# Optimization experiments

Hardware: AMD Instinct MI355X
Metric: run time of the kernel (lower is better)

The kernel has to match this reference:

```python
import math
import jax, jax.numpy as jnp
import numpy as np

BLOCK = 32          # hard-coded in the CUDA kernels
NUM_HEADS = 16
NUM_BLOCKS = 512    # (max_pos//32) * block_per_row = 128 * 4
DIAG_N = 3
FIRST_N = 0


def _mra2_attention(Q, K, V, mask):
    # Q,K,V: (meta_batch, seq, head_dim); mask: (meta_batch, seq) in {0,1}
    mb, seq_len, d = Q.shape
    bs = BLOCK
    nb = seq_len // bs
    scale = 1.0 / math.sqrt(d)
    Q = Q * mask[:, :, None]
    K = K * mask[:, :, None]
    V = V * mask[:, :, None]

    # ---- low resolution block means (mask-weighted), approx_mode='full' keeps V_hat
    tc = mask.reshape(mb, nb, bs).sum(-1)                 # token count per block
    denom = tc[:, :, None] + 1e-6
    Q_hat = Q.reshape(mb, nb, bs, d).sum(2) / denom       # (mb, nb, d)
    K_hat = K.reshape(mb, nb, bs, d).sum(2) / denom
    V_hat = V.reshape(mb, nb, bs, d).sum(2) / denom
    low_logit = jnp.einsum('bid,bjd->bij', Q_hat, K_hat) * scale
    row_max = low_logit.max(-1, keepdims=True)            # before mask subtraction
    low_logit = low_logit - 10000.0 * ((tc[:, None, :] * tc[:, :, None]) < 0.5).astype(Q.dtype)

    # ---- block index selection (torch runs this under no_grad)
    lrn = jax.lax.stop_gradient(low_logit - row_max)
    if DIAG_N > 0:
        off = DIAG_N // 2
        i = jnp.arange(nb)
        band = (jnp.abs(i[:, None] - i[None, :]) <= off).astype(Q.dtype)
        lrn = lrn + band[None] * 5000.0
    if FIRST_N > 0:
        lrn = lrn.at[:, :FIRST_N, :].add(5000.0)
        lrn = lrn.at[:, :, :FIRST_N].add(5000.0)
    top_vals, indices = jax.lax.top_k(lrn.reshape(mb, nb * nb), NUM_BLOCKS)
    threshold = top_vals.min(-1)
    high_mask = (lrn >= threshold[:, None, None]).astype(Q.dtype)  # selected-block mask

    q_blk = indices // nb                                  # (mb, n) query block ids
    k_blk = indices % nb                                   # (mb, n) key block ids
    Qs = jnp.take_along_axis(Q.reshape(mb, nb, bs, d), q_blk[:, :, None, None], axis=1)
    Ks = jnp.take_along_axis(K.reshape(mb, nb, bs, d), k_blk[:, :, None, None], axis=1)
    Vs = jnp.take_along_axis(V.reshape(mb, nb, bs, d), k_blk[:, :, None, None], axis=1)

    # sampled dense-dense: sparse_C[b,n,k,q] (key-in-block, query-in-block layout as in kernel)
    hi_logit = jnp.einsum('bnkd,bnqd->bnkq', Ks, Qs) * scale

    # per query-row max over selected blocks (kernel index_max; constant for grad)
    b_idx = jnp.arange(mb)[:, None]
    blk_max = hi_logit.max(axis=2)                         # (mb, n, bs) max over key axis
    max_blocks = jnp.full((mb, nb, bs), -1e8, Q.dtype).at[b_idx, q_blk].max(blk_max)
    max_blocks = jax.lax.stop_gradient(max_blocks)
    max_vals = max_blocks.reshape(mb, seq_len)
    max_scatter = jnp.take_along_axis(max_blocks, q_blk[:, :, None], axis=1)[:, :, None, :]

    # key-side mask per selected block (sparse_mask_B)
    mask_blk = jnp.take_along_axis(mask.reshape(mb, nb, bs), k_blk[:, :, None], axis=1)
    hi_attn = jnp.exp(hi_logit - max_scatter - 10000.0 * (1.0 - mask_blk[:, :, :, None]))

    # sparse-dense matmul + reduce-sum normalizer, scattered back per query block
    hi_out = jnp.zeros((mb, nb, bs, d), Q.dtype).at[b_idx, q_blk].add(
        jnp.einsum('bnkq,bnkd->bnqd', hi_attn, Vs)).reshape(mb, seq_len, d)
    hi_norm = jnp.zeros((mb, nb, bs), Q.dtype).at[b_idx, q_blk].add(
        hi_attn.sum(axis=2)).reshape(mb, seq_len)

    # ---- low resolution branch, selected blocks suppressed via high_mask
    low_attn = jnp.exp(low_logit - row_max - 10000.0 * high_mask) * tc[:, None, :]
    low_out = jnp.repeat(jnp.einsum('bij,bjd->bid', low_attn, V_hat), bs, axis=1)
    low_norm = jnp.repeat(low_attn.sum(-1), bs, axis=1)

    log_corr = (jnp.repeat(row_max[:, :, 0], bs, axis=1) - max_vals) * mask
    low_corr = jnp.exp(jnp.minimum(log_corr, 0.0))
    hi_corr = jnp.exp(-jnp.maximum(log_corr, 0.0))

    ctx = hi_out * hi_corr[:, :, None] + low_out * low_corr[:, :, None]
    ctx = ctx / (hi_norm * hi_corr + low_norm * low_corr + 1e-6)[:, :, None]
    return ctx * mask[:, :, None]


def _forward(hidden_states, attention_mask, w_q, b_q, w_k, b_k, w_v, b_v):
    b, s, hdim = hidden_states.shape
    h = NUM_HEADS
    dh = hdim // h

    def split_heads(x):
        return x.reshape(b, s, h, dh).transpose(0, 2, 1, 3).reshape(b * h, s, dh)

    q = split_heads(hidden_states @ w_q.T + b_q)
    k = split_heads(hidden_states @ w_k.T + b_k)
    v = split_heads(hidden_states @ w_v.T + b_v)
    # invert extended additive mask (1 + am/10000) and replicate over heads
    # (torch's .repeat(1, h, 1).reshape(b*h, s) stacks h copies of the [b,s] mask)
    mask = jnp.tile(1.0 + attention_mask / 10000.0, (h, 1))
    ctx = _mra2_attention(q, k, v, mask)
    ctx = ctx.reshape(b, h, s, dh).transpose(0, 2, 1, 3).reshape(b, s, hdim)
    return ctx


def setup_inputs() -> dict:
    key = jax.random.key(0)
    ks = jax.random.split(key, 4)
    H = 1024
    return {
        'hidden_states': jax.random.normal(ks[0], (2, 4096, H), jnp.float32),
        'attention_mask': jnp.zeros((2, 4096), jnp.float32),
        'w_q': jax.random.normal(ks[1], (H, H), jnp.float32) * 0.02,
        'b_q': jnp.zeros((H,), jnp.float32),
        'w_k': jax.random.normal(ks[2], (H, H), jnp.float32) * 0.02,
        'b_k': jnp.zeros((H,), jnp.float32),
        'w_v': jax.random.normal(ks[3], (H, H), jnp.float32) * 0.02,
        'b_v': jnp.zeros((H,), jnp.float32),
    }


def reference(hidden_states, attention_mask, w_q, b_q, w_k, b_k, w_v, b_v):
    return _forward(hidden_states, attention_mask, w_q, b_q, w_k, b_k, w_v, b_v)
```

## Files before the change

### kernel.cpp

```cpp
#include <hip/hip_runtime.h>
#include <cstdint>
#include <cstddef>

#define MAXSEL 160
static constexpr int S    = 4096;
static constexpr int H    = 1024;
static constexpr int DH   = 64;
static constexpr int NB   = 128;
static constexpr int MBH  = 32;
static constexpr int M8   = 8192;
static constexpr int N3   = 3072;

typedef _Float16 half8 __attribute__((ext_vector_type(8)));
typedef _Float16 half4v __attribute__((ext_vector_type(4)));
typedef float floatx4 __attribute__((ext_vector_type(4)));

__device__ __forceinline__ void load_lds16(const void* g, void* l) {
  __builtin_amdgcn_global_load_lds((const __attribute__((address_space(1))) unsigned int*)g,
                                   (__attribute__((address_space(3))) unsigned int*)l,
                                   16, 0, 0);
}

__global__ __launch_bounds__(256) void k_prep(const float* __restrict__ hidden,
                                              const float* __restrict__ am,
                                              const float* __restrict__ wq,
                                              const float* __restrict__ wk,
                                              const float* __restrict__ wv,
                                              _Float16* __restrict__ h16,
                                              _Float16* __restrict__ w16,
                                              _Float16* __restrict__ wlo,
                                              _Float16* __restrict__ hb_hi,
                                              _Float16* __restrict__ hb_lo,
                                              float* __restrict__ tcv,
                                              int* __restrict__ selcnt) {
  const int blk_id = blockIdx.x;
  if (blk_id < 256) {
    if (blk_id == 0) {
      for (int i = threadIdx.x; i < MBH * NB; i += 256) selcnt[i] = 0;
    }
    int b2 = blk_id >> 7, blk = blk_id & 127;
    int c = threadIdx.x * 4;
    float4 s0 = make_float4(0.f, 0.f, 0.f, 0.f);
    float4 s1 = make_float4(0.f, 0.f, 0.f, 0.f);
    for (int i = 0; i < 32; i += 4) {
      int pos0 = blk * 32 + i;
      size_t base = ((size_t)b2 * 4096 + pos0) * 1024 + c;
      const float4 x0 = *(const float4*)&hidden[base];
      const float4 x1 = *(const float4*)&hidden[base + 1024];
      const float4 x2 = *(const float4*)&hidden[base + 2048];
      const float4 x3 = *(const float4*)&hidden[base + 3072];
      float a00 = am[pos0],      a01 = am[pos0 + 1],      a02 = am[pos0 + 2],      a03 = am[pos0 + 3];
      float a10 = am[4096+pos0], a11 = am[4096+pos0 + 1], a12 = am[4096+pos0 + 2], a13 = am[4096+pos0 + 3];
      half4v h;
      h[0]=(_Float16)x0.x; h[1]=(_Float16)x0.y; h[2]=(_Float16)x0.z; h[3]=(_Float16)x0.w;
      *(half4v*)&h16[base] = h;
      h[0]=(_Float16)x1.x; h[1]=(_Float16)x1.y; h[2]=(_Float16)x1.z; h[3]=(_Float16)x1.w;
      *(half4v*)&h16[base + 1024] = h;
      h[0]=(_Float16)x2.x; h[1]=(_Float16)x2.y; h[2]=(_Float16)x2.z; h[3]=(_Float16)x2.w;
      *(half4v*)&h16[base + 2048] = h;
      h[0]=(_Float16)x3.x; h[1]=(_Float16)x3.y; h[2]=(_Float16)x3.z; h[3]=(_Float16)x3.w;
      *(half4v*)&h16[base + 3072] = h;
      float m0, m1;
      m0 = 1.f + a00 * 1e-4f; m1 = 1.f + a10 * 1e-4f;
      s0.x += m0*x0.x; s0.y += m0*x0.y; s0.z += m0*x0.z; s0.w += m0*x0.w;
      s1.x += m1*x0.x; s1.y += m1*x0.y; s1.z += m1*x0.z; s1.w += m1*x0.w;
      m0 = 1.f + a01 * 1e-4f; m1 = 1.f + a11 * 1e-4f;
      s0.x += m0*x1.x; s0.y += m0*x1.y; s0.z += m0*x1.z; s0.w += m0*x1.w;
      s1.x += m1*x1.x; s1.y += m1*x1.y; s1.z += m1*x1.z; s1.w += m1*x1.w;
      m0 = 1.f + a02 * 1e-4f; m1 = 1.f + a12 * 1e-4f;
      s0.x += m0*x2.x; s0.y += m0*x2.y; s0.z += m0*x2.z; s0.w += m0*x2.w;
      s1.x += m1*x2.x; s1.y += m1*x2.y; s1.z += m1*x2.z; s1.w += m1*x2.w;
      m0 = 1.f + a03 * 1e-4f; m1 = 1.f + a13 * 1e-4f;
      s0.x += m0*x3.x; s0.y += m0*x3.y; s0.z += m0*x3.z; s0.w += m0*x3.w;
      s1.x += m1*x3.x; s1.y += m1*x3.y; s1.z += m1*x3.z; s1.w += m1*x3.w;
    }
    size_t row0 = (size_t)(b2 * 2 + 0) * 128 + blk;
    size_t row1 = (size_t)(b2 * 2 + 1) * 128 + blk;
    half4v hi, lo;
    hi[0]=(_Float16)s0.x; lo[0]=(_Float16)(s0.x-(float)hi[0]);
    hi[1]=(_Float16)s0.y; lo[1]=(_Float16)(s0.y-(float)hi[1]);
    hi[2]=(_Float16)s0.z; lo[2]=(_Float16)(s0.z-(float)hi[2]);
    hi[3]=(_Float16)s0.w; lo[3]=(_Float16)(s0.w-(float)hi[3]);
    *(half4v*)&hb_hi[row0 * 1024 + c] = hi;
    *(half4v*)&hb_lo[row0 * 1024 + c] = lo;
    hi[0]=(_Float16)s1.x; lo[0]=(_Float16)(s1.x-(float)hi[0]);
    hi[1]=(_Float16)s1.y; lo[1]=(_Float16)(s1.y-(float)hi[1]);
    hi[2]=(_Float16)s1.z; lo[2]=(_Float16)(s1.z-(float)hi[2]);
    hi[3]=(_Float16)s1.w; lo[3]=(_Float16)(s1.w-(float)hi[3]);
    *(half4v*)&hb_hi[row1 * 1024 + c] = hi;
    *(half4v*)&hb_lo[row1 * 1024 + c] = lo;
    if (b2 == 0 && threadIdx.x == 0) {
      float t0 = 0.f, t1 = 0.f;
      for (int i = 0; i < 32; ++i) {
        int pos = blk * 32 + i;
        t0 += 1.f + am[pos] * 1e-4f;
        t1 += 1.f + am[4096 + pos] * 1e-4f;
      }
      tcv[blk] = t0; tcv[128 + blk] = t1;
    }
  } else {
    long j = (long)(blk_id - 256) * 256 + threadIdx.x;
    const long NW4 = (long)H * H / 4;
    int which = (int)(j / NW4);
    long jj = j - (long)which * NW4;
    const float* src = which == 0 ? wq : (which == 1 ? wk : wv);
    float4 x = ((const float4*)src)[jj];
    half4v h;
    h[0] = (_Float16)x.x; h[1] = (_Float16)x.y;
    h[2] = (_Float16)x.z; h[3] = (_Float16)x.w;
    *(half4v*)&w16[j * 4] = h;
    if (which < 2) {
      half4v r;
      r[0] = (_Float16)(x.x - (float)h[0]);
      r[1] = (_Float16)(x.y - (float)h[1]);
      r[2] = (_Float16)(x.z - (float)h[2]);
      r[3] = (_Float16)(x.w - (float)h[3]);
      *(half4v*)&wlo[j * 4] = r;
    }
  }
}

__global__ __launch_bounds__(256) void k_gemm_qkv(const _Float16* __restrict__ A,
                                                  const _Float16* __restrict__ B,
                                                  const float* __restrict__ bq,
                                                  const float* __restrict__ bk,
                                                  const float* __restrict__ bv,
                                                  const float* __restrict__ am,
                                                  _Float16* __restrict__ q16,
                                                  _Float16* __restrict__ k16,
                                                  _Float16* __restrict__ v16) {
  const int bx = blockIdx.x;
  const int by = blockIdx.y;
  const int tid = threadIdx.x;
  const int lane = tid & 63, wv = tid >> 6;
  const int wm = wv >> 1, wn = wv & 1;
  const int l15 = lane & 15, quad = lane >> 4;

  __shared__ _Float16 As[128 * 64];
  __shared__ _Float16 Bs[128 * 64];

  floatx4 acc[4][4] = {};

  const _Float16* Ag = A + (size_t)(by * 128) * 1024;
  const _Float16* Bg = B + (size_t)(bx * 128) * 1024;
  const int srow_l = lane >> 3;
  const int scol   = (((lane & 7) ^ (srow_l & 7)) * 8);
  const int swz    = l15 & 7;

  for (int k0 = 0; k0 < 1024; k0 += 64) {
    __syncthreads();
#pragma unroll
    for (int i = 0; i < 4; ++i) {
      int rb = i * 32 + wv * 8;
      load_lds16(Ag + (size_t)(rb + srow_l) * 1024 + k0 + scol, &As[rb * 64]);
      load_lds16(Bg + (size_t)(rb + srow_l) * 1024 + k0 + scol, &Bs[rb * 64]);
    }
    __syncthreads();
#pragma unroll
    for (int ks = 0; ks < 2; ++ks) {
      const int kc = ks * 4;
      half8 a[4], b[4];
#pragma unroll
      for (int mt = 0; mt < 4; ++mt)
        a[mt] = *(const half8*)&As[(wm * 64 + mt * 16 + l15) * 64 + (((kc + quad) ^ swz) << 3)];
#pragma unroll
      for (int nt = 0; nt < 4; ++nt)
        b[nt] = *(const half8*)&Bs[(wn * 64 + nt * 16 + l15) * 64 + (((kc + quad) ^ swz) << 3)];
#pragma unroll
      for (int mt = 0; mt < 4; ++mt)
#pragma unroll
        for (int nt = 0; nt < 4; ++nt)
          acc[mt][nt] = __builtin_amdgcn_mfma_f32_16x16x32_f16(a[mt], b[nt], acc[mt][nt], 0, 0, 0);
    }
  }

  const int which = (bx * 128) >> 10;
  const float* bias = which == 0 ? bq : (which == 1 ? bk : bv);
  _Float16* dst = which == 0 ? q16 : (which == 1 ? k16 : v16);
#pragma unroll
  for (int nt = 0; nt < 4; ++nt) {
    int o  = bx * 128 + wn * 64 + nt * 16 + l15;
    int oo = o & 1023;
    int hh = oo >> 6, dd = oo & 63;
    int m2 = hh & 1;
    float bsv = bias[oo];
#pragma unroll
    for (int mt = 0; mt < 4; ++mt) {
#pragma unroll
      for (int r = 0; r < 4; ++r) {
        int srow = by * 128 + wm * 64 + mt * 16 + quad * 4 + r;
        int b2 = srow >> 12, s = srow & 4095;
        float mv = 1.f + am[m2 * 4096 + s] * 1e-4f;
        float v = (acc[mt][nt][r] + bsv) * mv;
        int mb = b2 * 16 + hh;
        dst[((size_t)mb * 4096 + s) * 64 + dd] = (_Float16)v;
      }
    }
  }
}

__global__ __launch_bounds__(256) void k_sidev(const _Float16* __restrict__ Ahi,
                                               const _Float16* __restrict__ Alo,
                                               const _Float16* __restrict__ Bhi,
                                               const _Float16* __restrict__ Blo,
                                               float* __restrict__ sideQK,
                                               const _Float16* __restrict__ v16,
                                               const float* __restrict__ tcv,
                                               float* __restrict__ vhat,
                                               _Float16* __restrict__ v16T) {
  __shared__ _Float16 smem[4 * 64 * 64];
  const int tid = threadIdx.x;
  const int lane = tid & 63, wv = tid >> 6;

  if (blockIdx.x >= 512) {
    _Float16* Vs = &smem[wv * 2304];
    int bid = (blockIdx.x - 512) * 4 + wv;
    int mb = bid >> 7, blk = bid & 127;
    const _Float16* src = v16 + ((size_t)mb * 4096 + blk * 32) * 64;
    int r = lane >> 3, c = (lane & 7) * 8;
#pragma unroll
    for (int it = 0; it < 4; ++it)
      *(uint4*)&Vs[(it * 8 + r) * 72 + c] = *(const uint4*)&src[(it * 8 + r) * 64 + c];
    __syncthreads();
    float acc = 0.f;
    half8 col[4];
#pragma unroll
    for (int k = 0; k < 32; ++k) {
      _Float16 x = Vs[k * 72 + lane];
      col[k >> 3][k & 7] = x;
      acc += (float)x;
    }
    vhat[(size_t)bid * 64 + lane] = acc / (tcv[(mb & 1) * 128 + blk] + 1e-6f);
    _Float16* dst = v16T + (size_t)(mb * 64 + lane) * 4096 + blk * 32;
#pragma unroll
    for (int p = 0; p < 4; ++p) *(half8*)&dst[p * 8] = col[p];
    return;
  }

  const int kk = blockIdx.x >> 8;
  const int bb = blockIdx.x & 255;
  const int bx = bb & 31;
  const int by = bb >> 5;
  const int wm = wv >> 1, wn = wv & 1;
  const int l15 = lane & 15, quad = lane >> 4;
  _Float16* sAhi = smem;
  _Float16* sAlo = smem + 4096;
  _Float16* sBhi = smem + 8192;
  _Float16* sBlo = smem + 12288;

  floatx4 acc[2][2] = {};

  const int srow = lane >> 3;
  const int scol = (((lane & 7) ^ (srow & 7)) * 8);
  const int swz  = l15 & 7;
  const _Float16* src;
  _Float16* dst;
  if      (wv == 0) { src = Ahi + (size_t)(by * 64) * 1024; dst = sAhi; }
  else if (wv == 1) { src = Alo + (size_t)(by * 64) * 1024; dst = sAlo; }
  else if (wv == 2) { src = Bhi + (size_t)(bx * 64) * 1024; dst = sBhi; }
  else              { src = Blo + (size_t)(bx * 64) * 1024; dst = sBlo; }

  const int kbeg = kk * 512;
  for (int k0 = kbeg; k0 < kbeg + 512; k0 += 64) {
    __syncthreads();
#pragma unroll
    for (int i = 0; i < 8; ++i)
      load_lds16(src + (size_t)(i * 8 + srow) * 1024 + k0 + scol, dst + i * 512);
    __syncthreads();
#pragma unroll
    for (int ks = 0; ks < 2; ++ks) {
      const int kc = ks * 4;
      half8 ah[2], al[2], bh[2], bl[2];
#pragma unroll
      for (int mt = 0; mt < 2; ++mt) {
        int off = (wm * 32 + mt * 16 + l15) * 64 + (((kc + quad) ^ swz) << 3);
        ah[mt] = *(const half8*)&sAhi[off];
        al[mt] = *(const half8*)&sAlo[off];
      }
#pragma unroll
      for (int nt = 0; nt < 2; ++nt) {
        int off = (wn * 32 + nt * 16 + l15) * 64 + (((kc + quad) ^ swz) << 3);
        bh[nt] = *(const half8*)&sBhi[off];
        bl[nt] = *(const half8*)&sBlo[off];
      }
#pragma unroll
      for (int mt = 0; mt < 2; ++mt)
#pragma unroll
        for (int nt = 0; nt < 2; ++nt) {
          acc[mt][nt] = __builtin_amdgcn_mfma_f32_16x16x32_f16(ah[mt], bh[nt], acc[mt][nt], 0, 0, 0);
          acc[mt][nt] = __builtin_amdgcn_mfma_f32_16x16x32_f16(ah[mt], bl[nt], acc[mt][nt], 0, 0, 0);
          acc[mt][nt] = __builtin_amdgcn_mfma_f32_16x16x32_f16(al[mt], bh[nt], acc[mt][nt], 0, 0, 0);
        }
    }
  }
  float* outp = sideQK + (size_t)kk * (512 * 2048);
#pragma unroll
  for (int mt = 0; mt < 2; ++mt)
#pragma unroll
    for (int nt = 0; nt < 2; ++nt)
#pragma unroll
      for (int rr = 0; rr < 4; ++rr) {
        int row = by * 64 + wm * 32 + mt * 16 + quad * 4 + rr;
        int col = bx * 64 + wn * 32 + nt * 16 + l15;
        outp[(size_t)row * 2048 + col] = acc[mt][nt][rr];
      }
}

__global__ __launch_bounds__(256) void k_lowlogit(const float* __restrict__ sideQK,
                                                  const float* __restrict__ tcv,
                                                  const float* __restrict__ bq,
                                                  const float* __restrict__ bk,
                                                  float* __restrict__ ll,
                                                  float* __restrict__ rmaxout) {
  const int mb = blockIdx.x;
  const int ib = blockIdx.y;
  const int b2 = mb >> 4, m2 = mb & 1, hh = mb & 15;
  const int combo = b2 * 2 + m2;
  const int tid = threadIdx.x;
  __shared__ float Kh[128 * 64];
  __shared__ float Qh[16 * 64];
  __shared__ float tcL[128];

  const float* P1 = sideQK + (size_t)512 * 2048;

  if (tid < 128) tcL[tid] = tcv[m2 * 128 + tid];
  __syncthreads();
#pragma unroll
  for (int i = 0; i < 8; ++i) {
    int ci = tid + i * 256;
    int row = ci >> 4, c4 = (ci & 15) * 4;
    float tck = tcL[row];
    float den = 1.f / (tck + 1e-6f);
    size_t idx = ((size_t)combo * 128 + row) * 2048 + 1024 + hh * 64 + c4;
    float4 x0 = *(const float4*)&sideQK[idx];
    float4 x1 = *(const float4*)&P1[idx];
    float4 bb = *(const float4*)&bk[hh * 64 + c4];
    float4 o;
    o.x = (x0.x + x1.x + bb.x * tck) * den; o.y = (x0.y + x1.y + bb.y * tck) * den;
    o.z = (x0.z + x1.z + bb.z * tck) * den; o.w = (x0.w + x1.w + bb.w * tck) * den;
    *(float4*)&Kh[row * 64 + c4] = o;
  }
  {
    int row = tid >> 4, c4 = (tid & 15) * 4;
    int gi = ib * 16 + row;
    float tcq = tcL[gi];
    float den = 1.f / (tcq + 1e-6f);
    size_t idx = ((size_t)combo * 128 + gi) * 2048 + hh * 64 + c4;
    float4 x0 = *(const float4*)&sideQK[idx];
    float4 x1 = *(const float4*)&P1[idx];
    float4 bb = *(const float4*)&bq[hh * 64 + c4];
    float4 o;
    o.x = (x0.x + x1.x + bb.x * tcq) * den; o.y = (x0.y + x1.y + bb.y * tcq) * den;
    o.z = (x0.z + x1.z + bb.z * tcq) * den; o.w = (x0.w + x1.w + bb.w * tcq) * den;
    *(float4*)&Qh[row * 64 + c4] = o;
  }
  __syncthreads();

  const int il = tid >> 4, jg = tid & 15;
  const int i = ib * 16 + il;
  float tcq = tcL[i];
  float dots[8] = {};
#pragma unroll
  for (int dd = 0; dd < 16; ++dd) {
    int d4 = ((dd + tid) & 15) * 4;
    float4 qv = *(const float4*)&Qh[il * 64 + d4];
#pragma unroll
    for (int jj = 0; jj < 8; ++jj) {
      float4 kv = *(const float4*)&Kh[(jg * 8 + jj) * 64 + d4];
      dots[jj] += qv.x * kv.x + qv.y * kv.y + qv.z * kv.z + qv.w * kv.w;
    }
  }
  float tmax = -1e30f;
#pragma unroll
  for (int jj = 0; jj < 8; ++jj) {
    int j = jg * 8 + jj;
    float raw = dots[jj] * 0.125f;
    tmax = fmaxf(tmax, raw);
    float pen = (tcq * tcL[j] < 0.5f) ? 10000.f : 0.f;
    ll[(size_t)mb * 16384 + (size_t)i * 128 + j] = raw - pen;
  }
#pragma unroll
  for (int mk = 1; mk < 16; mk <<= 1) tmax = fmaxf(tmax, __shfl_xor(tmax, mk));
  if (jg == 0) rmaxout[mb * 128 + i] = tmax;
}

__global__ __launch_bounds__(256) void k_topk(const float* __restrict__ ll,
                                              const float* __restrict__ rmax,
                                              float* __restrict__ thr,
                                              int* __restrict__ selcnt,
                                              int* __restrict__ selkb) {
  const int mb = blockIdx.x;
  const int t = threadIdx.x;
  const int wid = t >> 6;
  __shared__ int red2[2][4];

  unsigned code[64];
#pragma unroll
  for (int j = 0; j < 64; ++j) {
    int e = j * 256 + t;
    int i = e >> 7, jj = e & 127;
    float lrn = ll[(size_t)mb * 16384 + e] - rmax[mb * 128 + i];
    int di = i - jj;
    if (di <= 1 && di >= -1) lrn += 5000.f;
    unsigned b = __float_as_uint(lrn);
    code[j] = (b & 0x80000000u) ? ~b : (b | 0x80000000u);
  }

  unsigned lo = 0u, hi = 0xFFFFFFFFu;
  for (int it = 0; it < 32; ++it) {
    unsigned mid = lo + ((hi - lo) >> 1);
    int c = 0;
#pragma unroll
    for (int j = 0; j < 64; ++j) c += (code[j] >= mid) ? 1 : 0;
#pragma unroll
    for (int mk = 1; mk < 64; mk <<= 1) c += __shfl_xor(c, mk);
    if ((t & 63) == 0) red2[it & 1][wid] = c;
    __syncthreads();
    int total = red2[it & 1][0] + red2[it & 1][1] + red2[it & 1][2] + red2[it & 1][3];
    if (total >= 512) lo = mid; else hi = mid;
  }
  if (t == 0) {
    unsigned bits = (lo & 0x80000000u) ? (lo & 0x7FFFFFFFu) : ~lo;
    thr[mb] = __uint_as_float(bits);
  }
#pragma unroll
  for (int j = 0; j < 64; ++j) {
    if (code[j] >= lo) {
      int e = j * 256 + t;
      int i = e >> 7, jj = e & 127;
      int slot = atomicAdd(&selcnt[mb * 128 + i], 1);
      if (slot < MAXSEL) selkb[(size_t)(mb * 128 + i) * MAXSEL + slot] = jj;
    }
  }
}

__global__ __launch_bounds__(64) void k_hi(const _Float16* __restrict__ q16,
                                           const _Float16* __restrict__ k16,
                                           const _Float16* __restrict__ v16T,
                                           const int* __restrict__ selcnt,
                                           const int* __restrict__ selkb,
                                           const float* __restrict__ rmax,
                                           const float* __restrict__ thr,
                                           const float* __restrict__ tcv,
                                           const float* __restrict__ vhat,
                                           const float* __restrict__ ll,
                                           const float* __restrict__ am,
                                           float* __restrict__ out) {
  const int mb = blockIdx.x & 31, qb = blockIdx.x >> 5;
  const int sid = mb * 128 + qb;
  const int lane = threadIdx.x;
  const int l15 = lane & 15, quad = lane >> 4;
  const int m2 = mb & 1, b2 = mb >> 4, hh = mb & 15;

  __shared__ _Float16 Ps[32 * 40];

  const _Float16* qbase = q16 + ((size_t)mb * 4096 + qb * 32) * 64;
  half8 aq[2][2];
#pragma unroll
  for (int mt = 0; mt < 2; ++mt)
#pragma unroll
    for (int ks = 0; ks < 2; ++ks)
      aq[mt][ks] = *(const half8*)&qbase[(mt * 16 + l15) * 64 + ks * 32 + quad * 8];

  const float rmaxb = rmax[sid];
  const float th = thr[mb];
  float accL = 0.f, nrmL = 0.f;
#pragma unroll 4
  for (int j = 0; j < 128; ++j) {
    float llv = ll[(size_t)mb * 16384 + (size_t)qb * 128 + j];
    float lrn = llv - rmaxb;
    int di = qb - j;
    if (di <= 1 && di >= -1) lrn += 5000.f;
    float w = (lrn >= th) ? 0.f : __expf(llv - rmaxb) * tcv[m2 * 128 + j];
    accL += w * vhat[((size_t)(mb * 128 + j)) * 64 + lane];
    nrmL += w;
  }

  int nk = selcnt[sid];
  if (nk > MAXSEL) nk = MAXSEL;
  const int* list = selkb + (size_t)sid * MAXSEL;

  const _Float16* kbase  = k16  + (size_t)mb * 4096 * 64;
  const _Float16* vtbase = v16T + (size_t)mb * 64 * 4096;

  float rm[2][4];
  floatx4 o[2][4] = {};
  floatx4 onrm[2] = {};
#pragma unroll
  for (int mt = 0; mt < 2; ++mt)
#pragma unroll
    for (int r = 0; r < 4; ++r) rm[mt][r] = -1e8f;

  half8 ones;
#pragma unroll
  for (int j = 0; j < 8; ++j) ones[j] = (_Float16)1.f;

  for (int t = 0; t < nk; ++t) {
    const int kb = list[t];
    const _Float16* kp = kbase + (size_t)kb * 32 * 64;
    half8 b0[2], b1[2];
#pragma unroll
    for (int ks = 0; ks < 2; ++ks) {
      b0[ks] = *(const half8*)&kp[(l15) * 64 + ks * 32 + quad * 8];
      b1[ks] = *(const half8*)&kp[(16 + l15) * 64 + ks * 32 + quad * 8];
    }
    const _Float16* vp = vtbase + kb * 32 + quad * 8;
    half8 vb0 = *(const half8*)&vp[(size_t)(l15) * 4096];
    half8 vb1 = *(const half8*)&vp[(size_t)(16 + l15) * 4096];
    half8 vb2 = *(const half8*)&vp[(size_t)(32 + l15) * 4096];
    half8 vb3 = *(const half8*)&vp[(size_t)(48 + l15) * 4096];

    floatx4 sf[2][2] = {};
    sf[0][0] = __builtin_amdgcn_mfma_f32_16x16x32_f16(aq[0][0], b0[0], sf[0][0], 0, 0, 0);
    sf[0][0] = __builtin_amdgcn_mfma_f32_16x16x32_f16(aq[0][1], b0[1], sf[0][0], 0, 0, 0);
    sf[0][1] = __builtin_amdgcn_mfma_f32_16x16x32_f16(aq[0][0], b1[0], sf[0][1], 0, 0, 0);
    sf[0][1] = __builtin_amdgcn_mfma_f32_16x16x32_f16(aq[0][1], b1[1], sf[0][1], 0, 0, 0);
    sf[1][0] = __builtin_amdgcn_mfma_f32_16x16x32_f16(aq[1][0], b0[0], sf[1][0], 0, 0, 0);
    sf[1][0] = __builtin_amdgcn_mfma_f32_16x16x32_f16(aq[1][1], b0[1], sf[1][0], 0, 0, 0);
    sf[1][1] = __builtin_amdgcn_mfma_f32_16x16x32_f16(aq[1][0], b1[0], sf[1][1], 0, 0, 0);
    sf[1][1] = __builtin_amdgcn_mfma_f32_16x16x32_f16(aq[1][1], b1[1], sf[1][1], 0, 0, 0);

    float pen0, pen1;
    {
      float mk0 = 1.f + am[m2 * 4096 + kb * 32 + l15] * 1e-4f;
      float mk1 = 1.f + am[m2 * 4096 + kb * 32 + 16 + l15] * 1e-4f;
      pen0 = 10000.f * (1.f - mk0);
      pen1 = 10000.f * (1.f - mk1);
    }
#pragma unroll
    for (int mt = 0; mt < 2; ++mt)
#pragma unroll
      for (int r = 0; r < 4; ++r) {
        float s0 = sf[mt][0][r] * 0.125f;
        float s1 = sf[mt][1][r] * 0.125f;
        float v = fmaxf(s0, s1);
#pragma unroll
        for (int mk = 1; mk < 16; mk <<= 1) v = fmaxf(v, __shfl_xor(v, mk));
        float mnew  = fmaxf(rm[mt][r], v);
        float alpha = __expf(rm[mt][r] - mnew);
        rm[mt][r] = mnew;
        float p0 = __expf(s0 - mnew - pen0);
        float p1 = __expf(s1 - mnew - pen1);
        o[mt][0][r] *= alpha; o[mt][1][r] *= alpha;
        o[mt][2][r] *= alpha; o[mt][3][r] *= alpha;
        onrm[mt][r] *= alpha;
        int row = mt * 16 + quad * 4 + r;
        Ps[row * 40 + l15] = (_Float16)p0;
        Ps[row * 40 + 16 + l15] = (_Float16)p1;
      }
    __syncthreads();
    half8 pa0 = *(const half8*)&Ps[(l15) * 40 + quad * 8];
    half8 pa1 = *(const half8*)&Ps[(16 + l15) * 40 + quad * 8];
    o[0][0] = __builtin_amdgcn_mfma_f32_16x16x32_f16(pa0, vb0, o[0][0], 0, 0, 0);
    o[0][1] = __builtin_amdgcn_mfma_f32_16x16x32_f16(pa0, vb1, o[0][1], 0, 0, 0);
    o[0][2] = __builtin_amdgcn_mfma_f32_16x16x32_f16(pa0, vb2, o[0][2], 0, 0, 0);
    o[0][3] = __builtin_amdgcn_mfma_f32_16x16x32_f16(pa0, vb3, o[0][3], 0, 0, 0);
    o[1][0] = __builtin_amdgcn_mfma_f32_16x16x32_f16(pa1, vb0, o[1][0], 0, 0, 0);
    o[1][1] = __builtin_amdgcn_mfma_f32_16x16x32_f16(pa1, vb1, o[1][1], 0, 0, 0);
    o[1][2] = __builtin_amdgcn_mfma_f32_16x16x32_f16(pa1, vb2, o[1][2], 0, 0, 0);
    o[1][3] = __builtin_amdgcn_mfma_f32_16x16x32_f16(pa1, vb3, o[1][3], 0, 0, 0);
    onrm[0] = __builtin_amdgcn_mfma_f32_16x16x32_f16(pa0, ones, onrm[0], 0, 0, 0);
    onrm[1] = __builtin_amdgcn_mfma_f32_16x16x32_f16(pa1, ones, onrm[1], 0, 0, 0);
    __syncthreads();
  }

  float lo_d[4];
#pragma unroll
  for (int ntd = 0; ntd < 4; ++ntd) lo_d[ntd] = __shfl(accL, ntd * 16 + l15);
#pragma unroll
  for (int mt = 0; mt < 2; ++mt) {
#pragma unroll
    for (int r = 0; r < 4; ++r) {
      int q = mt * 16 + quad * 4 + r;
      int qpos = qb * 32 + q;
      float mq = 1.f + am[m2 * 4096 + qpos] * 1e-4f;
      float logc = (rmaxb - rm[mt][r]) * mq;
      float lc = __expf(fminf(logc, 0.f));
      float hc = __expf(-fmaxf(logc, 0.f));
      float den = onrm[mt][r] * hc + nrmL * lc + 1e-6f;
      float sc = mq / den;
#pragma unroll
      for (int ntd = 0; ntd < 4; ++ntd) {
        float val = (o[mt][ntd][r] * hc + lo_d[ntd] * lc) * sc;
        out[((size_t)b2 * 4096 + qpos) * 1024 + hh * 64 + ntd * 16 + l15] = val;
      }
    }
  }
}

extern "C" void kernel_launch(void* const* d_in, const int* in_sizes, int n_in,
                              void* d_out, int out_size, void* d_ws, size_t ws_size,
                              hipStream_t stream) {
  const float* hidden = (const float*)d_in[0];
  const float* am     = (const float*)d_in[1];
  const float* wq     = (const float*)d_in[2];
  const float* bq     = (const float*)d_in[3];
  const float* wk     = (const float*)d_in[4];
  const float* bk     = (const float*)d_in[5];
  const float* wv     = (const float*)d_in[6];
  const float* bv     = (const float*)d_in[7];
  float* out = (float*)d_out;

  char* ws = (char*)d_ws;
  size_t off = 0;
  auto alloc = [&](size_t bytes) -> char* {
    char* p = ws + off;
    off += (bytes + 255) & ~(size_t)255;
    return p;
  };
  _Float16* h16    = (_Float16*)alloc((size_t)M8 * H * 2);
  _Float16* w16    = (_Float16*)alloc((size_t)N3 * H * 2);
  _Float16* wlo    = (_Float16*)alloc((size_t)2 * H * H * 2);
  _Float16* q16    = (_Float16*)alloc((size_t)MBH * S * DH * 2);
  _Float16* k16    = (_Float16*)alloc((size_t)MBH * S * DH * 2);
  _Float16* v16    = (_Float16*)alloc((size_t)MBH * S * DH * 2);
  _Float16* hb_hi  = (_Float16*)alloc((size_t)4 * NB * H * 2);
  _Float16* hb_lo  = (_Float16*)alloc((size_t)4 * NB * H * 2);
  float* tcv       = (float*)alloc((size_t)2 * NB * 4);
  float* sideQK    = (float*)alloc((size_t)2 * 512 * 2048 * 4);
  float* ll        = (float*)alloc((size_t)MBH * NB * NB * 4);
  float* rmax      = (float*)alloc((size_t)MBH * NB * 4);
  float* thr       = (float*)alloc((size_t)MBH * 4);
  int*   selcnt    = (int*)alloc((size_t)MBH * NB * 4);
  int*   selkb     = (int*)alloc((size_t)MBH * NB * MAXSEL * 4);
  float* vhat      = (float*)alloc((size_t)MBH * NB * DH * 4);
  _Float16* v16T   = h16;

  k_prep<<<dim3(3328), dim3(256), 0, stream>>>(hidden, am, wq, wk, wv,
                                               h16, w16, wlo, hb_hi, hb_lo, tcv, selcnt);
  k_gemm_qkv<<<dim3(24, 64), dim3(256), 0, stream>>>(h16, w16, bq, bk, bv, am,
                                                     q16, k16, v16);
  k_sidev<<<dim3(512 + 1024), dim3(256), 0, stream>>>(hb_hi, hb_lo, w16, wlo, sideQK,
                                                      v16, tcv, vhat, v16T);
  k_lowlogit<<<dim3(32, 8), dim3(256), 0, stream>>>(sideQK, tcv, bq, bk, ll, rmax);
  k_topk<<<dim3(32), dim3(256), 0, stream>>>(ll, rmax, thr, selcnt, selkb);
  k_hi<<<dim3(4096), dim3(64), 0, stream>>>(q16, k16, v16T, selcnt, selkb, rmax, thr,
                                            tcv, vhat, ll, am, out);
}
```

Baseline: 304.4 us.

## Double-buffer QKV GEMM with 128x256 tiles, 8 waves and swizzled block order

Rewrites the QKV projection GEMM to use 512-thread blocks computing 128x256 output tiles, with double-buffered LDS so the next K-tile's global-to-LDS loads overlap the current tile's MFMAs. It adds a linear block-id remap that groups blocks for L2 reuse, and uses s_setprio around the MFMA bursts. The aim is to hide global load latency and raise arithmetic intensity per block. In exchange it uses more LDS per block (96 KB), which limits occupancy, and it relies on hand-placed barriers and waitcnts for correctness.

```diff
diff --git a/kernel.cpp b/kernel.cpp
--- a/kernel.cpp
+++ b/kernel.cpp
@@ -120,70 +120,133 @@
   }
 }
 
-__global__ __launch_bounds__(256) void k_gemm_qkv(const _Float16* __restrict__ A,
-                                                  const _Float16* __restrict__ B,
-                                                  const float* __restrict__ bq,
-                                                  const float* __restrict__ bk,
-                                                  const float* __restrict__ bv,
-                                                  const float* __restrict__ am,
-                                                  _Float16* __restrict__ q16,
-                                                  _Float16* __restrict__ k16,
-                                                  _Float16* __restrict__ v16) {
-  const int bx = blockIdx.x;
-  const int by = blockIdx.y;
+__global__ __launch_bounds__(512, 2) void k_gemm_qkv(const _Float16* __restrict__ A,
+                                                     const _Float16* __restrict__ B,
+                                                     const float* __restrict__ bq,
+                                                     const float* __restrict__ bk,
+                                                     const float* __restrict__ bv,
+                                                     const float* __restrict__ am,
+                                                     _Float16* __restrict__ q16,
+                                                     _Float16* __restrict__ k16,
+                                                     _Float16* __restrict__ v16) {
+  const int id = blockIdx.x;
+  const int swz = (id & 7) * 96 + (id >> 3);
+  const int by = swz / 12;
+  const int bx = swz - by * 12;
   const int tid = threadIdx.x;
   const int lane = tid & 63, wv = tid >> 6;
-  const int wm = wv >> 1, wn = wv & 1;
+  const int wm = wv >> 2, wn = wv & 3;
   const int l15 = lane & 15, quad = lane >> 4;
 
-  __shared__ _Float16 As[128 * 64];
-  __shared__ _Float16 Bs[128 * 64];
+  __shared__ _Float16 As[2][128 * 64];
+  __shared__ _Float16 Bs[2][256 * 64];
 
   floatx4 acc[4][4] = {};
 
   const _Float16* Ag = A + (size_t)(by * 128) * 1024;
-  const _Float16* Bg = B + (size_t)(bx * 128) * 1024;
+  const _Float16* Bg = B + (size_t)(bx * 256) * 1024;
   const int srow_l = lane >> 3;
-  const int scol   = (((lane & 7) ^ (srow_l & 7)) * 8);
-  const int swz    = l15 & 7;
-
-  for (int k0 = 0; k0 < 1024; k0 += 64) {
-    __syncthreads();
-#pragma unroll
-    for (int i = 0; i < 4; ++i) {
-      int rb = i * 32 + wv * 8;
-      load_lds16(Ag + (size_t)(rb + srow_l) * 1024 + k0 + scol, &As[rb * 64]);
-      load_lds16(Bg + (size_t)(rb + srow_l) * 1024 + k0 + scol, &Bs[rb * 64]);
-    }
-    __syncthreads();
-#pragma unroll
-    for (int ks = 0; ks < 2; ++ks) {
-      const int kc = ks * 4;
-      half8 a[4], b[4];
-#pragma unroll
-      for (int mt = 0; mt < 4; ++mt)
-        a[mt] = *(const half8*)&As[(wm * 64 + mt * 16 + l15) * 64 + (((kc + quad) ^ swz) << 3)];
-#pragma unroll
-      for (int nt = 0; nt < 4; ++nt)
-        b[nt] = *(const half8*)&Bs[(wn * 64 + nt * 16 + l15) * 64 + (((kc + quad) ^ swz) << 3)];
-#pragma unroll
-      for (int mt = 0; mt < 4; ++mt)
-#pragma unroll
-        for (int nt = 0; nt < 4; ++nt)
-          acc[mt][nt] = __builtin_amdgcn_mfma_f32_16x16x32_f16(a[mt], b[nt], acc[mt][nt], 0, 0, 0);
-    }
-  }
-
-  const int which = (bx * 128) >> 10;
+  const int scol   = ((lane & 7) ^ srow_l) * 8;
+  const int swzr   = l15 & 7;
+
+  const int arb = wv * 16;
+  const int brb = wv * 32;
+
+  {
+    const _Float16* ag = Ag + (size_t)(arb + srow_l) * 1024 + scol;
+    const _Float16* bg = Bg + (size_t)(brb + srow_l) * 1024 + scol;
+#pragma unroll
+    for (int i = 0; i < 2; ++i)
+      load_lds16(ag + (size_t)i * 8 * 1024, &As[0][(arb + i * 8) * 64]);
+#pragma unroll
+    for (int i = 0; i < 4; ++i)
+      load_lds16(bg + (size_t)i * 8 * 1024, &Bs[0][(brb + i * 8) * 64]);
+  }
+  asm volatile("s_waitcnt vmcnt(0)" ::: "memory");
+  __builtin_amdgcn_s_barrier();
+
+#define KTILE(T, CUR)                                                                     \
+  {                                                                                       \
+                             \
+    if ((T) < 15) {                                                                       \
+      const int kn = ((T) + 1) * 64;                                                      \
+      const _Float16* ag = Ag + (size_t)(arb + srow_l) * 1024 + kn + scol;                \
+      const _Float16* bg = Bg + (size_t)(brb + srow_l) * 1024 + kn + scol;                \
+      _Pragma("unroll")                                                                   \
+      for (int i = 0; i < 2; ++i)                                                         \
+        load_lds16(ag + (size_t)i * 8 * 1024, &As[(CUR) ^ 1][(arb + i * 8) * 64]);        \
+      _Pragma("unroll")                                                                   \
+      for (int i = 0; i < 4; ++i)                                                         \
+        load_lds16(bg + (size_t)i * 8 * 1024, &Bs[(CUR) ^ 1][(brb + i * 8) * 64]);        \
+    }                                                                                     \
+    half8 a[2][2], b[4][2];                                                               \
+                                          \
+    _Pragma("unroll")                                                                     \
+    for (int nt = 0; nt < 4; ++nt)                                                        \
+      _Pragma("unroll")                                                                   \
+      for (int ks = 0; ks < 2; ++ks)                                                      \
+        b[nt][ks] = *(const half8*)&Bs[CUR][(wn * 64 + nt * 16 + l15) * 64 +              \
+                                            (((ks * 4 + quad) ^ swzr) << 3)];             \
+    _Pragma("unroll")                                                                     \
+    for (int mt = 0; mt < 2; ++mt)                                                        \
+      _Pragma("unroll")                                                                   \
+      for (int ks = 0; ks < 2; ++ks)                                                      \
+        a[mt][ks] = *(const half8*)&As[CUR][(wm * 64 + mt * 16 + l15) * 64 +              \
+                                            (((ks * 4 + quad) ^ swzr) << 3)];             \
+    __builtin_amdgcn_s_barrier();                                                         \
+    asm volatile("s_waitcnt lgkmcnt(0)" ::: "memory");                                    \
+    __builtin_amdgcn_s_setprio(1);                                                        \
+    _Pragma("unroll")                                                                     \
+    for (int mt = 0; mt < 2; ++mt)                                                        \
+      _Pragma("unroll")                                                                   \
+      for (int nt = 0; nt < 4; ++nt) {                                                    \
+        acc[mt][nt] = __builtin_amdgcn_mfma_f32_16x16x32_f16(a[mt][0], b[nt][0],          \
+                                                             acc[mt][nt], 0, 0, 0);       \
+        acc[mt][nt] = __builtin_amdgcn_mfma_f32_16x16x32_f16(a[mt][1], b[nt][1],          \
+                                                             acc[mt][nt], 0, 0, 0);       \
+      }                                                                                   \
+    __builtin_amdgcn_s_setprio(0);                                                        \
+    __builtin_amdgcn_s_barrier();                                                         \
+                                             \
+    _Pragma("unroll")                                                                     \
+    for (int mt = 0; mt < 2; ++mt)                                                        \
+      _Pragma("unroll")                                                                   \
+      for (int ks = 0; ks < 2; ++ks)                                                      \
+        a[mt][ks] = *(const half8*)&As[CUR][(wm * 64 + (mt + 2) * 16 + l15) * 64 +        \
+                                            (((ks * 4 + quad) ^ swzr) << 3)];             \
+    __builtin_amdgcn_s_barrier();                                                         \
+    asm volatile("s_waitcnt lgkmcnt(0)" ::: "memory");                                    \
+    __builtin_amdgcn_s_setprio(1);                                                        \
+    _Pragma("unroll")                                                                     \
+    for (int mt = 0; mt < 2; ++mt)                                                        \
+      _Pragma("unroll")                                                                   \
+      for (int nt = 0; nt < 4; ++nt) {                                                    \
+        acc[mt + 2][nt] = __builtin_amdgcn_mfma_f32_16x16x32_f16(a[mt][0], b[nt][0],      \
+                                                                 acc[mt + 2][nt], 0, 0, 0);\
+        acc[mt + 2][nt] = __builtin_amdgcn_mfma_f32_16x16x32_f16(a[mt][1], b[nt][1],      \
+                                                                 acc[mt + 2][nt], 0, 0, 0);\
+      }                                                                                   \
+    __builtin_amdgcn_s_setprio(0);                                                        \
+               \
+    if ((T) < 15) asm volatile("s_waitcnt vmcnt(0)" ::: "memory");                        \
+    __builtin_amdgcn_s_barrier();                                                         \
+  }
+
+  for (int t2 = 0; t2 < 8; ++t2) {
+    KTILE(2 * t2,     0)
+    KTILE(2 * t2 + 1, 1)
+  }
+#undef KTILE
+
+  const int which = bx >> 2;
   const float* bias = which == 0 ? bq : (which == 1 ? bk : bv);
   _Float16* dst = which == 0 ? q16 : (which == 1 ? k16 : v16);
+  const int hh = (bx & 3) * 4 + wn;
+  const int m2 = hh & 1;
 #pragma unroll
   for (int nt = 0; nt < 4; ++nt) {
-    int o  = bx * 128 + wn * 64 + nt * 16 + l15;
-    int oo = o & 1023;
-    int hh = oo >> 6, dd = oo & 63;
-    int m2 = hh & 1;
-    float bsv = bias[oo];
+    const int dd = nt * 16 + l15;
+    const float bsv = bias[hh * 64 + dd];
 #pragma unroll
     for (int mt = 0; mt < 4; ++mt) {
 #pragma unroll
@@ -628,8 +691,8 @@
 
   k_prep<<<dim3(3328), dim3(256), 0, stream>>>(hidden, am, wq, wk, wv,
                                                h16, w16, wlo, hb_hi, hb_lo, tcv, selcnt);
-  k_gemm_qkv<<<dim3(24, 64), dim3(256), 0, stream>>>(h16, w16, bq, bk, bv, am,
-                                                     q16, k16, v16);
+  k_gemm_qkv<<<dim3(768), dim3(512), 0, stream>>>(h16, w16, bq, bk, bv, am,
+                                                  q16, k16, v16);
   k_sidev<<<dim3(512 + 1024), dim3(256), 0, stream>>>(hb_hi, hb_lo, w16, wlo, sideQK,
                                                       v16, tcv, vhat, v16T);
   k_lowlogit<<<dim3(32, 8), dim3(256), 0, stream>>>(sideQK, tcv, bq, bk, ll, rmax);
```

Result: slower. 318.0 us (+4.5%).

## Pipeline QKV GEMM with triple-buffered LDS, larger N tile and XCD swizzle

Applied to the files above, without the earlier changes.

Rewrites the QKV projection GEMM to use 512-thread blocks with 128x256 tiles and a K-step of 32. Global-to-LDS loads are triple-buffered, with partial vmcnt waits and a single barrier per step, so loads overlap MFMA work. It also adds a block-index swizzle for cache locality and raises wave priority around the MFMAs. This is meant to hide memory latency that the old single-buffered loop with two barriers per step exposed, at the cost of more LDS use and more complex synchronisation.

```diff
diff --git a/kernel.cpp b/kernel.cpp
--- a/kernel.cpp
+++ b/kernel.cpp
@@ -120,70 +120,89 @@
   }
 }
 
-__global__ __launch_bounds__(256) void k_gemm_qkv(const _Float16* __restrict__ A,
-                                                  const _Float16* __restrict__ B,
-                                                  const float* __restrict__ bq,
-                                                  const float* __restrict__ bk,
-                                                  const float* __restrict__ bv,
-                                                  const float* __restrict__ am,
-                                                  _Float16* __restrict__ q16,
-                                                  _Float16* __restrict__ k16,
-                                                  _Float16* __restrict__ v16) {
-  const int bx = blockIdx.x;
-  const int by = blockIdx.y;
+__global__ __launch_bounds__(512, 4) void k_gemm_qkv(const _Float16* __restrict__ A,
+                                                     const _Float16* __restrict__ B,
+                                                     const float* __restrict__ bq,
+                                                     const float* __restrict__ bk,
+                                                     const float* __restrict__ bv,
+                                                     const float* __restrict__ am,
+                                                     _Float16* __restrict__ q16,
+                                                     _Float16* __restrict__ k16,
+                                                     _Float16* __restrict__ v16) {
+  const int id = blockIdx.x;
+  const int swz = (id & 7) * 96 + (id >> 3);
+  const int by = swz / 12;
+  const int bx = swz - by * 12;
   const int tid = threadIdx.x;
   const int lane = tid & 63, wv = tid >> 6;
-  const int wm = wv >> 1, wn = wv & 1;
+  const int wm = wv >> 2, wn = wv & 3;
   const int l15 = lane & 15, quad = lane >> 4;
 
-  __shared__ _Float16 As[128 * 64];
-  __shared__ _Float16 Bs[128 * 64];
+  __shared__ _Float16 As[3][128 * 32];
+  __shared__ _Float16 Bs[3][256 * 32];
 
   floatx4 acc[4][4] = {};
 
   const _Float16* Ag = A + (size_t)(by * 128) * 1024;
-  const _Float16* Bg = B + (size_t)(bx * 128) * 1024;
-  const int srow_l = lane >> 3;
-  const int scol   = (((lane & 7) ^ (srow_l & 7)) * 8);
-  const int swz    = l15 & 7;
-
-  for (int k0 = 0; k0 < 1024; k0 += 64) {
-    __syncthreads();
-#pragma unroll
-    for (int i = 0; i < 4; ++i) {
-      int rb = i * 32 + wv * 8;
-      load_lds16(Ag + (size_t)(rb + srow_l) * 1024 + k0 + scol, &As[rb * 64]);
-      load_lds16(Bg + (size_t)(rb + srow_l) * 1024 + k0 + scol, &Bs[rb * 64]);
-    }
-    __syncthreads();
-#pragma unroll
-    for (int ks = 0; ks < 2; ++ks) {
-      const int kc = ks * 4;
-      half8 a[4], b[4];
-#pragma unroll
-      for (int mt = 0; mt < 4; ++mt)
-        a[mt] = *(const half8*)&As[(wm * 64 + mt * 16 + l15) * 64 + (((kc + quad) ^ swz) << 3)];
+  const _Float16* Bg = B + (size_t)(bx * 256) * 1024;
+
+  const int gr  = lane >> 2;
+  const int gcb = ((lane & 3) ^ ((lane >> 3) & 3)) * 8;
+  const _Float16* agl  = Ag + (size_t)(wv * 16 + gr) * 1024 + gcb;
+  const _Float16* bgl0 = Bg + (size_t)(wv * 32 + gr) * 1024 + gcb;
+  const _Float16* bgl1 = Bg + (size_t)(wv * 32 + 16 + gr) * 1024 + gcb;
+  const int aw  = (wv * 16) * 32;
+  const int bw0 = (wv * 32) * 32;
+  const int bw1 = (wv * 32 + 16) * 32;
+
+#define STAGE(TT, BB)                                          \
+  {                                                            \
+    load_lds16(agl  + (size_t)(TT) * 32, &As[BB][aw]);         \
+    load_lds16(bgl0 + (size_t)(TT) * 32, &Bs[BB][bw0]);        \
+    load_lds16(bgl1 + (size_t)(TT) * 32, &Bs[BB][bw1]);        \
+  }
+
+  STAGE(0, 0)
+  STAGE(1, 1)
+
+  const int rc = ((quad ^ ((l15 >> 1) & 3)) << 3);
+
+#pragma unroll
+  for (int t = 0; t < 32; ++t) {
+    if (t == 31) { asm volatile("s_waitcnt vmcnt(0)" ::: "memory"); }
+    else         { asm volatile("s_waitcnt vmcnt(3)" ::: "memory"); }
+    __builtin_amdgcn_s_barrier();
+    if (t < 30) {
+      const int nb = (t + 2) % 3;
+      STAGE(t + 2, nb)
+    }
+    const int bb = t % 3;
+    half8 a[4], b[4];
+#pragma unroll
+    for (int mt = 0; mt < 4; ++mt)
+      a[mt] = *(const half8*)&As[bb][(wm * 64 + mt * 16 + l15) * 32 + rc];
+#pragma unroll
+    for (int nt = 0; nt < 4; ++nt)
+      b[nt] = *(const half8*)&Bs[bb][(wn * 64 + nt * 16 + l15) * 32 + rc];
+    __builtin_amdgcn_s_setprio(1);
+#pragma unroll
+    for (int mt = 0; mt < 4; ++mt)
 #pragma unroll
       for (int nt = 0; nt < 4; ++nt)
-        b[nt] = *(const half8*)&Bs[(wn * 64 + nt * 16 + l15) * 64 + (((kc + quad) ^ swz) << 3)];
-#pragma unroll
-      for (int mt = 0; mt < 4; ++mt)
-#pragma unroll
-        for (int nt = 0; nt < 4; ++nt)
-          acc[mt][nt] = __builtin_amdgcn_mfma_f32_16x16x32_f16(a[mt], b[nt], acc[mt][nt], 0, 0, 0);
-    }
-  }
-
-  const int which = (bx * 128) >> 10;
+        acc[mt][nt] = __builtin_amdgcn_mfma_f32_16x16x32_f16(a[mt], b[nt], acc[mt][nt], 0, 0, 0);
+    __builtin_amdgcn_s_setprio(0);
+  }
+#undef STAGE
+
+  const int which = bx >> 2;
   const float* bias = which == 0 ? bq : (which == 1 ? bk : bv);
   _Float16* dst = which == 0 ? q16 : (which == 1 ? k16 : v16);
+  const int hh = (bx & 3) * 4 + wn;
+  const int m2 = hh & 1;
 #pragma unroll
   for (int nt = 0; nt < 4; ++nt) {
-    int o  = bx * 128 + wn * 64 + nt * 16 + l15;
-    int oo = o & 1023;
-    int hh = oo >> 6, dd = oo & 63;
-    int m2 = hh & 1;
-    float bsv = bias[oo];
+    const int dd = nt * 16 + l15;
+    const float bsv = bias[hh * 64 + dd];
 #pragma unroll
     for (int mt = 0; mt < 4; ++mt) {
 #pragma unroll
@@ -628,8 +647,8 @@
 
   k_prep<<<dim3(3328), dim3(256), 0, stream>>>(hidden, am, wq, wk, wv,
                                                h16, w16, wlo, hb_hi, hb_lo, tcv, selcnt);
-  k_gemm_qkv<<<dim3(24, 64), dim3(256), 0, stream>>>(h16, w16, bq, bk, bv, am,
-                                                     q16, k16, v16);
+  k_gemm_qkv<<<dim3(768), dim3(512), 0, stream>>>(h16, w16, bq, bk, bv, am,
+                                                  q16, k16, v16);
   k_sidev<<<dim3(512 + 1024), dim3(256), 0, stream>>>(hb_hi, hb_lo, w16, wlo, sideQK,
                                                       v16, tcv, vhat, v16T);
   k_lowlogit<<<dim3(32, 8), dim3(256), 0, stream>>>(sideQK, tcv, bq, bk, ll, rmax);
```

Result: no change. 307.9 us (+1.2%).

## Triple-buffer QKV GEMM with 256x128 tiles, 8 waves and grouped block swizzle

Applied to the files above, without the earlier changes.

Rewrites the fp16 QKV projection GEMM to use 512-thread blocks computing 256x128 output tiles, a three-stage LDS ring buffer with async global-to-LDS loads issued two k-tiles ahead and split across two half-phases, and explicit waitcnt/barrier/setprio scheduling. The grid becomes a 1D launch remapped so that groups of blocks share A/B tiles in L2. The goal is to hide global load latency behind MFMA work and to improve data reuse, at the cost of more LDS (~144KB per block) and fragile hand-scheduled synchronisation.

```diff
diff --git a/kernel.cpp b/kernel.cpp
--- a/kernel.cpp
+++ b/kernel.cpp
@@ -120,75 +120,111 @@
   }
 }
 
-__global__ __launch_bounds__(256) void k_gemm_qkv(const _Float16* __restrict__ A,
-                                                  const _Float16* __restrict__ B,
-                                                  const float* __restrict__ bq,
-                                                  const float* __restrict__ bk,
-                                                  const float* __restrict__ bv,
-                                                  const float* __restrict__ am,
-                                                  _Float16* __restrict__ q16,
-                                                  _Float16* __restrict__ k16,
-                                                  _Float16* __restrict__ v16) {
-  const int bx = blockIdx.x;
-  const int by = blockIdx.y;
+__global__ __launch_bounds__(512, 2) void k_gemm_qkv(const _Float16* __restrict__ A,
+                                                     const _Float16* __restrict__ B,
+                                                     const float* __restrict__ bq,
+                                                     const float* __restrict__ bk,
+                                                     const float* __restrict__ bv,
+                                                     const float* __restrict__ am,
+                                                     _Float16* __restrict__ q16,
+                                                     _Float16* __restrict__ k16,
+                                                     _Float16* __restrict__ v16) {
+  const int id = blockIdx.x;
+  const int swz = (id & 7) * 96 + (id >> 3);
+  const int by = swz / 24;
+  const int bx = swz - by * 24;
   const int tid = threadIdx.x;
   const int lane = tid & 63, wv = tid >> 6;
   const int wm = wv >> 1, wn = wv & 1;
   const int l15 = lane & 15, quad = lane >> 4;
 
-  __shared__ _Float16 As[128 * 64];
-  __shared__ _Float16 Bs[128 * 64];
+  __shared__ _Float16 As[3][256 * 64];
+  __shared__ _Float16 Bs[3][128 * 64];
 
   floatx4 acc[4][4] = {};
 
-  const _Float16* Ag = A + (size_t)(by * 128) * 1024;
+  const _Float16* Ag = A + (size_t)(by * 256) * 1024;
   const _Float16* Bg = B + (size_t)(bx * 128) * 1024;
-  const int srow_l = lane >> 3;
-  const int scol   = (((lane & 7) ^ (srow_l & 7)) * 8);
-  const int swz    = l15 & 7;
-
-  for (int k0 = 0; k0 < 1024; k0 += 64) {
-    __syncthreads();
-#pragma unroll
-    for (int i = 0; i < 4; ++i) {
-      int rb = i * 32 + wv * 8;
-      load_lds16(Ag + (size_t)(rb + srow_l) * 1024 + k0 + scol, &As[rb * 64]);
-      load_lds16(Bg + (size_t)(rb + srow_l) * 1024 + k0 + scol, &Bs[rb * 64]);
-    }
-    __syncthreads();
-#pragma unroll
-    for (int ks = 0; ks < 2; ++ks) {
-      const int kc = ks * 4;
-      half8 a[4], b[4];
-#pragma unroll
-      for (int mt = 0; mt < 4; ++mt)
-        a[mt] = *(const half8*)&As[(wm * 64 + mt * 16 + l15) * 64 + (((kc + quad) ^ swz) << 3)];
-#pragma unroll
-      for (int nt = 0; nt < 4; ++nt)
-        b[nt] = *(const half8*)&Bs[(wn * 64 + nt * 16 + l15) * 64 + (((kc + quad) ^ swz) << 3)];
-#pragma unroll
-      for (int mt = 0; mt < 4; ++mt)
-#pragma unroll
-        for (int nt = 0; nt < 4; ++nt)
-          acc[mt][nt] = __builtin_amdgcn_mfma_f32_16x16x32_f16(a[mt], b[nt], acc[mt][nt], 0, 0, 0);
-    }
-  }
-
-  const int which = (bx * 128) >> 10;
+
+  const int gr  = lane >> 3;
+  const int gcb = ((lane & 7) ^ gr) * 8;
+  const _Float16* agl = Ag + (size_t)(wv * 32 + gr) * 1024 + gcb;
+  const _Float16* bgl = Bg + (size_t)(wv * 16 + gr) * 1024 + gcb;
+  const int aw = (wv * 32) * 64;
+  const int bw = (wv * 16) * 64;
+
+#define STAGE_P0(TT, BB)                                                   \
+  {                                                                        \
+    load_lds16(agl + (size_t)(TT) * 64,                 &As[BB][aw]);      \
+    load_lds16(agl + (size_t)(TT) * 64 + 8 * 1024,      &As[BB][aw + 512]);\
+    load_lds16(bgl + (size_t)(TT) * 64,                 &Bs[BB][bw]);      \
+  }
+#define STAGE_P1(TT, BB)                                                   \
+  {                                                                        \
+    load_lds16(agl + (size_t)(TT) * 64 + 16 * 1024,     &As[BB][aw + 1024]);\
+    load_lds16(agl + (size_t)(TT) * 64 + 24 * 1024,     &As[BB][aw + 1536]);\
+    load_lds16(bgl + (size_t)(TT) * 64 + 8 * 1024,      &Bs[BB][bw + 512]);\
+  }
+
+  STAGE_P0(0, 0) STAGE_P1(0, 0)
+  STAGE_P0(1, 1) STAGE_P1(1, 1)
+
+  const int rg0 = ((quad    ) ^ (l15 & 7)) << 3;
+  const int rg1 = ((quad ^ 4) ^ (l15 & 7)) << 3;
+
+#define PHASE(RG, STAGE_STMT)                                                         \
+  {                                                                                   \
+    half8 a[4], b[4];                                                                 \
+    _Pragma("unroll")                                                                 \
+    for (int mt = 0; mt < 4; ++mt)                                                    \
+      a[mt] = *(const half8*)&As[bb][(wm * 64 + mt * 16 + l15) * 64 + (RG)];          \
+    _Pragma("unroll")                                                                 \
+    for (int nt = 0; nt < 4; ++nt)                                                    \
+      b[nt] = *(const half8*)&Bs[bb][(wn * 64 + nt * 16 + l15) * 64 + (RG)];          \
+    STAGE_STMT                                                                        \
+    __builtin_amdgcn_s_barrier();                                                     \
+    asm volatile("s_waitcnt lgkmcnt(0)" ::: "memory");                                \
+    __builtin_amdgcn_s_setprio(1);                                                    \
+    _Pragma("unroll")                                                                 \
+    for (int mt = 0; mt < 4; ++mt)                                                    \
+      _Pragma("unroll")                                                               \
+      for (int nt = 0; nt < 4; ++nt)                                                  \
+        acc[mt][nt] = __builtin_amdgcn_mfma_f32_16x16x32_f16(a[mt], b[nt],            \
+                                                             acc[mt][nt], 0, 0, 0);   \
+    __builtin_amdgcn_s_setprio(0);                                                    \
+  }
+
+#pragma unroll
+  for (int t = 0; t < 16; ++t) {
+    if (t < 15) { asm volatile("s_waitcnt vmcnt(6)" ::: "memory"); }
+    else        { asm volatile("s_waitcnt vmcnt(0)" ::: "memory"); }
+    __builtin_amdgcn_s_barrier();
+    const int bb = t % 3;
+    const int nbuf = (t + 2) % 3;
+    if (t < 14) { PHASE(rg0, STAGE_P0(t + 2, nbuf)) }
+    else        { PHASE(rg0, ) }
+    __builtin_amdgcn_s_barrier();
+    if (t < 14) { PHASE(rg1, STAGE_P1(t + 2, nbuf)) }
+    else        { PHASE(rg1, ) }
+  }
+#undef PHASE
+#undef STAGE_P0
+#undef STAGE_P1
+
+  const int which = bx >> 3;
   const float* bias = which == 0 ? bq : (which == 1 ? bk : bv);
   _Float16* dst = which == 0 ? q16 : (which == 1 ? k16 : v16);
+  const int hh = (bx & 7) * 2 + wn;
+  const int m2 = hh & 1;
 #pragma unroll
   for (int nt = 0; nt < 4; ++nt) {
-    int o  = bx * 128 + wn * 64 + nt * 16 + l15;
-    int oo = o & 1023;
-    int hh = oo >> 6, dd = oo & 63;
-    int m2 = hh & 1;
-    float bsv = bias[oo];
+    const int dd = nt * 16 + l15;
+    const float bsv = bias[hh * 64 + dd];
 #pragma unroll
     for (int mt = 0; mt < 4; ++mt) {
 #pragma unroll
       for (int r = 0; r < 4; ++r) {
-        int srow = by * 128 + wm * 64 + mt * 16 + quad * 4 + r;
+        int srow = by * 256 + wm * 64 + mt * 16 + quad * 4 + r;
         int b2 = srow >> 12, s = srow & 4095;
         float mv = 1.f + am[m2 * 4096 + s] * 1e-4f;
         float v = (acc[mt][nt][r] + bsv) * mv;
@@ -628,8 +664,8 @@
 
   k_prep<<<dim3(3328), dim3(256), 0, stream>>>(hidden, am, wq, wk, wv,
                                                h16, w16, wlo, hb_hi, hb_lo, tcv, selcnt);
-  k_gemm_qkv<<<dim3(24, 64), dim3(256), 0, stream>>>(h16, w16, bq, bk, bv, am,
-                                                     q16, k16, v16);
+  k_gemm_qkv<<<dim3(768), dim3(512), 0, stream>>>(h16, w16, bq, bk, bv, am,
+                                                  q16, k16, v16);
   k_sidev<<<dim3(512 + 1024), dim3(256), 0, stream>>>(hb_hi, hb_lo, w16, wlo, sideQK,
                                                       v16, tcv, vhat, v16T);
   k_lowlogit<<<dim3(32, 8), dim3(256), 0, stream>>>(sideQK, tcv, bq, bk, ll, rmax);
```

Result: no change. 304.1 us (-0.1%).
